# Kernel optimization log

Hardware: AMD Instinct MI355X
Metric: run time of the kernel (lower is better)

## Reference

```python
import jax, jax.numpy as jnp
import numpy as np

H = 4                      # attention heads
N_A, N_P = 20000, 30000    # author / paper node counts
E = 200000                 # edges per edge type
IN, HID, OUT = 256, 256, 128
NEG_SLOPE = 0.2


def setup_inputs() -> dict:
    key = jax.random.key(0)
    ks = jax.random.split(key, 24)

    def w(k, shape, fan_in):
        return jax.random.normal(k, shape, jnp.float32) / np.float32(np.sqrt(fan_in))

    inp = {
        'x_author': jax.random.normal(ks[0], (N_A, IN), jnp.float32),
        'x_paper':  jax.random.normal(ks[1], (N_P, IN), jnp.float32),
        'src_ap': jax.random.randint(ks[2], (E,), 0, N_A, jnp.int32),
        'dst_ap': jax.random.randint(ks[3], (E,), 0, N_P, jnp.int32),
        'src_pa': jax.random.randint(ks[4], (E,), 0, N_P, jnp.int32),
        'dst_pa': jax.random.randint(ks[5], (E,), 0, N_A, jnp.int32),
        'src_pp': jax.random.randint(ks[6], (E,), 0, N_P, jnp.int32),
        'dst_pp': jax.random.randint(ks[7], (E,), 0, N_P, jnp.int32),
        'src_aa': jax.random.randint(ks[8], (E,), 0, N_A, jnp.int32),
        'dst_aa': jax.random.randint(ks[9], (E,), 0, N_A, jnp.int32),
        # layer 1 params
        'W1_a': w(ks[10], (IN, HID), IN), 'b1_a': jnp.zeros((HID,), jnp.float32),
        'W1_p': w(ks[11], (IN, HID), IN), 'b1_p': jnp.zeros((HID,), jnp.float32),
        'att1_src': w(ks[12], (4, H, HID // H), HID // H),
        'att1_dst': w(ks[13], (4, H, HID // H), HID // H),
        'q1': w(ks[14], (HID,), HID),
        'k1_W': w(ks[15], (HID, HID), HID), 'k1_b': jnp.zeros((HID,), jnp.float32),
        # layer 2 params
        'W2_a': w(ks[16], (HID, OUT), HID), 'b2_a': jnp.zeros((OUT,), jnp.float32),
        'W2_p': w(ks[17], (HID, OUT), HID), 'b2_p': jnp.zeros((OUT,), jnp.float32),
        'att2_src': w(ks[18], (4, H, OUT // H), OUT // H),
        'att2_dst': w(ks[19], (4, H, OUT // H), OUT // H),
        'q2': w(ks[20], (OUT,), OUT),
        'k2_W': w(ks[21], (OUT, OUT), OUT), 'k2_b': jnp.zeros((OUT,), jnp.float32),
    }
    return inp


def _han_layer(h, edges, att_src, att_dst, q, kW, kb, sizes):
    """One HANConv layer. h: dict node_type -> [N, H, D]."""
    outs = {nt: [] for nt in h}
    for i, (st, dt, row, col) in enumerate(edges):
        xs, xd = h[st], h[dt]
        nd = sizes[dt]
        # per-edge additive attention logits  [E, H]
        a = jax.nn.leaky_relu((xs * att_src[i]).sum(-1)[row]
                              + (xd * att_dst[i]).sum(-1)[col], NEG_SLOPE)
        # softmax over incoming edges of each dst node (segment softmax)
        amax = jax.ops.segment_max(a, col, num_segments=nd)
        ea = jnp.exp(a - amax[col])
        denom = jax.ops.segment_sum(ea, col, num_segments=nd)
        alpha = ea / (denom[col] + 1e-16)
        # weighted scatter-sum of source features  [Nd, H, D]
        agg = jax.ops.segment_sum(xs[row] * alpha[:, :, None], col, num_segments=nd)
        outs[dt].append(jax.nn.relu(agg.reshape(nd, -1)))
    # semantic (metapath-level) attention: PyG group()
    res = {}
    for nt, lst in outs.items():
        stk = jnp.stack(lst)  # [M, N, F]
        score = (q * jnp.tanh(stk @ kW + kb).mean(axis=1)).sum(-1)  # [M]
        attn = jax.nn.softmax(score, axis=0)
        res[nt] = jnp.einsum('m,mnf->nf', attn, stk)
    return res


def reference(x_author, x_paper, src_ap, dst_ap, src_pa, dst_pa, src_pp, dst_pp,
              src_aa, dst_aa, W1_a, b1_a, W1_p, b1_p, att1_src, att1_dst, q1,
              k1_W, k1_b, W2_a, b2_a, W2_p, b2_p, att2_src, att2_dst, q2,
              k2_W, k2_b):
    sizes = {'author': N_A, 'paper': N_P}
    edges = [('author', 'paper', src_ap, dst_ap),
             ('paper', 'author', src_pa, dst_pa),
             ('paper', 'paper', src_pp, dst_pp),
             ('author', 'author', src_aa, dst_aa)]
    d1 = W1_a.shape[1] // H
    h1 = {'author': (x_author @ W1_a + b1_a).reshape(N_A, H, d1),
          'paper':  (x_paper @ W1_p + b1_p).reshape(N_P, H, d1)}
    x1 = _han_layer(h1, edges, att1_src, att1_dst, q1, k1_W, k1_b, sizes)
    d2 = W2_a.shape[1] // H
    h2 = {'author': (x1['author'] @ W2_a + b2_a).reshape(N_A, H, d2),
          'paper':  (x1['paper'] @ W2_p + b2_p).reshape(N_P, H, d2)}
    x2 = _han_layer(h2, edges, att2_src, att2_dst, q2, k2_W, k2_b, sizes)
    return x2['author']
```

## Files before the change

kernel.cpp:

```cpp
#include <hip/hip_runtime.h>
#include <math.h>


#define NA 20000
#define NP 30000
#define NE 200000
#define D1 256
#define D2 128

typedef __attribute__((ext_vector_type(8))) short short8v;
typedef __attribute__((ext_vector_type(4))) float floatx4;
typedef __attribute__((ext_vector_type(8))) unsigned short ushort8v;
typedef __attribute__((ext_vector_type(4))) unsigned short ushort4v;

static __device__ __forceinline__ float lrelu(float x) { return x >= 0.f ? x : 0.2f * x; }

static __device__ __forceinline__ unsigned short bftrunc(float x) {
    return (unsigned short)(__float_as_uint(x) >> 16);
}
static __device__ __forceinline__ float bf2f(unsigned short b) {
    return __uint_as_float(((unsigned)b) << 16);
}
static __device__ __forceinline__ unsigned short bfrn(float x) {
    unsigned u = __float_as_uint(x);
    return (unsigned short)((u + 0x7FFFu + ((u >> 16) & 1u)) >> 16);
}

typedef __attribute__((address_space(1))) const unsigned int as1_uint;
typedef __attribute__((address_space(3))) unsigned int as3_uint;
static __device__ __forceinline__ void gl_lds16(const void* g, void* l) {
    __builtin_amdgcn_global_load_lds((as1_uint*)g, (as3_uint*)l, 16, 0, 0);
}

static inline int cdiv(int a, int b) { return (a + b - 1) / b; }

struct Prologue {
    const float* W[6];
    unsigned short* img[6];
    int N[6];
    int nsl[6];
    const float* x[2];
    unsigned short* xo[2];
    int xn8[2];
    const int* dstv[4];
    int* cnt[4];
};

__global__ __launch_bounds__(256) void prologue_k(Prologue p) {
    const int task = blockIdx.y;
    const int idx = blockIdx.x * 256 + threadIdx.x;
    if (task < 6) {
        const int m = task;
        if (idx >= p.nsl[m]) return;
        const int N = p.N[m];
        const int slot = idx & 3;
        const int col = (idx >> 2) % N;
        const int rest = (idx >> 2) / N;
        const int part = rest & 1;
        const int kt = rest >> 1;
        const int ks = slot ^ ((col >> 1) & 3);
        unsigned short* dst = p.img[m] + (((size_t)(kt * 2 + part) * N + col) * 32) + slot * 8;
        const float* wsrc = p.W[m] + (size_t)(kt * 32 + ks * 8) * N + col;
        short8v o;
#pragma unroll
        for (int k = 0; k < 8; ++k) {
            const float x = wsrc[(size_t)k * N];
            const unsigned short hb = bftrunc(x);
            o[k] = part ? (short)bftrunc(x - bf2f(hb)) : (short)hb;
        }
        *(short8v*)dst = o;
    } else if (task < 8) {
        const int m = task - 6;
        if (idx >= p.xn8[m]) return;
        const float* xp = p.x[m] + (size_t)idx * 8;
        float4 v0 = *(const float4*)xp;
        float4 v1 = *(const float4*)(xp + 4);
        const float xs8[8] = {v0.x, v0.y, v0.z, v0.w, v1.x, v1.y, v1.z, v1.w};
        short8v o;
#pragma unroll
        for (int k = 0; k < 8; ++k) o[k] = (short)bfrn(xs8[k]);
        *(short8v*)&p.xo[m][(size_t)idx * 8] = o;
    } else {
        const int ty = task - 8;
        if (idx < NE) atomicAdd(&p.cnt[ty][p.dstv[ty][idx]], 1);
    }
}

struct CsrBatch {
    const int* srcv[4];
    const int* dstv[4];
    int* cnt[4];
    int* csrc[4];
    int* cdst[4];
};

__global__ __launch_bounds__(256) void fill_csr_b(CsrBatch c, int n) {
    const int ty = blockIdx.y;
    const int i = blockIdx.x * 256 + threadIdx.x;
    if (i < n) {
        const int d = c.dstv[ty][i];
        const int p = atomicAdd(&c.cnt[ty][d], 1);
        c.csrc[ty][p] = c.srcv[ty][i];
        c.cdst[ty][p] = d;
    }
}

__global__ __launch_bounds__(1024) void exscan4(int* __restrict__ curbase,
                                                int* __restrict__ rpbase) {
    const int off_c[4] = {0, NP, NP + NA, NP + NA + NP};
    const int off_r[4] = {0, NP + 1, NP + NA + 2, NP + NA + NP + 3};
    const int ns[4] = {NP, NA, NP, NA};
    const int b = blockIdx.x;
    int* cur = curbase + off_c[b];
    int* rp = rpbase + off_r[b];
    const int n = ns[b];
    __shared__ int wsum[16];
    __shared__ int carry_s;
    const int t = threadIdx.x, wv = t >> 6, ln = t & 63;
    if (t == 0) carry_s = 0;
    __syncthreads();
    for (int base = 0; base < n; base += 1024) {
        const int i = base + t;
        const int v = (i < n) ? cur[i] : 0;
        int x = v;
#pragma unroll
        for (int off = 1; off < 64; off <<= 1) {
            int y = __shfl_up(x, off);
            if (ln >= off) x += y;
        }
        if (ln == 63) wsum[wv] = x;
        __syncthreads();
        if (wv == 0) {
            int s = (ln < 16) ? wsum[ln] : 0;
#pragma unroll
            for (int off = 1; off < 16; off <<= 1) {
                int y = __shfl_up(s, off);
                if (ln >= off) s += y;
            }
            if (ln < 16) wsum[ln] = s;
        }
        __syncthreads();
        const int woff = (wv == 0) ? 0 : wsum[wv - 1];
        const int c = carry_s;
        const int ex = c + woff + x - v;
        if (i < n) { rp[i] = ex; cur[i] = ex; }
        __syncthreads();
        if (t == 1023) carry_s = c + wsum[15];
        __syncthreads();
    }
    if (t == 0) rp[n] = carry_s;
}

template <int NT>
struct GemmBatch {
    const unsigned short* A[NT];
    const unsigned short* Wimg[NT];
    const float* bias[NT];
    unsigned short* C[NT];
    int M[NT];
};

template <int BN, bool SCORE, bool SPLITW, int NT>
__global__ __launch_bounds__(256) void gemm_sw(
    GemmBatch<NT> g, const float* __restrict__ qv, float* __restrict__ score, int K) {
    constexpr int WGN = BN / 64;
    constexpr int WGM = 4 / WGN;
    constexpr int BM = WGM * 64;
    constexpr int NB = SPLITW ? 2 : 1;
    constexpr int ACH = BM * 32 * 2 / 1024;
    constexpr int BCH = NB * BN * 32 * 2 / 1024;
    constexpr int CPW = (ACH + BCH) / 4;
    constexpr int ASZ = BM * 64;
    constexpr int BSZ = NB * BN * 64;
    const int ty = blockIdx.y;
    const int M = g.M[ty];
    const int bm = blockIdx.x * BM;
    if (bm >= M) return;
    const unsigned short* __restrict__ A = g.A[ty];
    const unsigned short* __restrict__ Wi = g.Wimg[ty];
    const float* __restrict__ bias = g.bias[ty];
    __shared__ __attribute__((aligned(16))) unsigned short As[2][BM][32];
    __shared__ __attribute__((aligned(16))) unsigned short Bs[2][NB][BN][32];
    const int t = threadIdx.x;
    const int lane = t & 63, wid = t >> 6;
    const int wr = wid / WGN, wc = wid % WGN;
    const int fq = lane >> 4, fr = lane & 15;
    const int asl = (fq ^ ((fr >> 1) & 3)) * 16;
    const int lr = lane >> 2;
    const int lks = (lane & 3) ^ ((lane >> 3) & 3);
    floatx4 acc[4][4];
#pragma unroll
    for (int i = 0; i < 4; ++i)
#pragma unroll
        for (int j = 0; j < 4; ++j) acc[i][j] = {0.f, 0.f, 0.f, 0.f};

    const int NK = K >> 5;
    auto STAGE = [&](int b, int ki) {
        const char* wbase = (const char*)Wi + (size_t)ki * (2 * BN * 64);
#pragma unroll
        for (int ci = 0; ci < CPW; ++ci) {
            const int c = wid * CPW + ci;
            if (c < ACH) {
                const int row = c * 16 + lr;
                const char* srcp = (const char*)(A + (size_t)(bm + row) * K + ki * 32 + lks * 8);
                gl_lds16(srcp, (char*)As + b * ASZ + c * 1024);
            } else {
                const int bc = c - ACH;
                gl_lds16(wbase + (size_t)bc * 1024 + lane * 16, (char*)Bs + b * BSZ + bc * 1024);
            }
        }
    };
    STAGE(0, 0);
    __syncthreads();
    int cur = 0;
    for (int ki = 0; ki < NK; ++ki) {
        if (ki + 1 < NK) STAGE(cur ^ 1, ki + 1);
        short8v a[4], bh[4], bl[4];
#pragma unroll
        for (int f = 0; f < 4; ++f) {
            const int ar = wr * 64 + f * 16 + fr;
            a[f] = *(const short8v*)((const char*)As + cur * ASZ + ar * 64 + asl);
            const int bc = wc * 64 + f * 16 + fr;
            bh[f] = *(const short8v*)((const char*)Bs + cur * BSZ + bc * 64 + asl);
            if constexpr (SPLITW)
                bl[f] = *(const short8v*)((const char*)Bs + cur * BSZ + (size_t)BN * 64 + bc * 64 + asl);
        }
#pragma unroll
        for (int i = 0; i < 4; ++i)
#pragma unroll
            for (int j = 0; j < 4; ++j) {
                acc[i][j] = __builtin_amdgcn_mfma_f32_16x16x32_bf16(a[i], bh[j], acc[i][j], 0, 0, 0);
                if constexpr (SPLITW)
                    acc[i][j] = __builtin_amdgcn_mfma_f32_16x16x32_bf16(a[i], bl[j], acc[i][j], 0, 0, 0);
            }
        __syncthreads();
        cur ^= 1;
    }
    if constexpr (!SCORE) {
        unsigned short* __restrict__ Cb = g.C[ty];
#pragma unroll
        for (int i = 0; i < 4; ++i) {
            const int gr0 = bm + wr * 64 + i * 16 + fq * 4;
#pragma unroll
            for (int j = 0; j < 4; ++j) {
                const int col = wc * 64 + j * 16 + fr;
                const float b = bias[col];
#pragma unroll
                for (int r = 0; r < 4; ++r) {
                    const int gr = gr0 + r;
                    if (gr < M) Cb[(size_t)gr * BN + col] = bfrn(acc[i][j][r] + b);
                }
            }
        }
    } else {
        __shared__ float red[256];
        float partial = 0.f;
#pragma unroll
        for (int i = 0; i < 4; ++i) {
            const int gr0 = bm + wr * 64 + i * 16 + fq * 4;
#pragma unroll
            for (int j = 0; j < 4; ++j) {
                const int col = wc * 64 + j * 16 + fr;
                const float b = bias[col], q = qv[col];
#pragma unroll
                for (int r = 0; r < 4; ++r) {
                    if (gr0 + r < M) partial += tanhf(acc[i][j][r] + b) * q;
                }
            }
        }
        red[t] = partial;
        __syncthreads();
        for (int s = 128; s > 0; s >>= 1) {
            if (t < s) red[t] += red[t + s];
            __syncthreads();
        }
        if (t == 0) atomicAdd(&score[ty], red[0]);
    }
}

struct NsBatch {
    const unsigned short* hx[2];
    const float* att[2][4];
    float* out[2][4];
    int n[2];
    int nsc[2];
};

template <int HD>
__global__ __launch_bounds__(256) void ns_b(NsBatch p) {
    const int ty = blockIdx.y;
    const int idx = blockIdx.x * 256 + threadIdx.x;
    const int node = idx >> 2, hh = idx & 3;
    if (node >= p.n[ty]) return;
    const unsigned short* row = p.hx[ty] + (size_t)node * (4 * HD) + hh * HD;
    const int nsc = p.nsc[ty];
    float s[4] = {0.f, 0.f, 0.f, 0.f};
#pragma unroll
    for (int d = 0; d < HD; d += 4) {
        ushort4v xv = *(const ushort4v*)&row[d];
        const float x0 = bf2f(xv[0]), x1 = bf2f(xv[1]), x2 = bf2f(xv[2]), x3 = bf2f(xv[3]);
#pragma unroll
        for (int v = 0; v < 4; ++v) {
            if (v < nsc) {
                float4 a = *(const float4*)&p.att[ty][v][hh * HD + d];
                s[v] += x0 * a.x + x1 * a.y + x2 * a.z + x3 * a.w;
            }
        }
    }
#pragma unroll
    for (int v = 0; v < 4; ++v)
        if (v < nsc) p.out[ty][v][idx] = s[v];
}

template <int EPL>
static __device__ __forceinline__ void accum(const unsigned short* p, float ea, float* acc) {
    if constexpr (EPL >= 8) {
#pragma unroll
        for (int w = 0; w < EPL / 8; ++w) {
            ushort8v x = *(const ushort8v*)(p + w * 8);
#pragma unroll
            for (int k = 0; k < 8; ++k) acc[w * 8 + k] += bf2f(x[k]) * ea;
        }
    } else {
        ushort4v x = *(const ushort4v*)p;
#pragma unroll
        for (int k = 0; k < 4; ++k) acc[k] += bf2f(x[k]) * ea;
    }
}

template <int NT>
struct AggBatch {
    const unsigned short* xs[NT];
    const float* ss[NT];
    const float* sd[NT];
    const int* csrc[NT];
    const int* rowptr[NT];
    unsigned short* out[NT];
    int ndst[NT];
};

template <int D, int NT>
__global__ __launch_bounds__(256) void agg_b(AggBatch<NT> a) {
    constexpr int EPL = D / 32;
    const int ty = blockIdx.y;
    const int gid = blockIdx.x * 8 + (threadIdx.x >> 5);
    if (gid >= a.ndst[ty]) return;
    const int g = threadIdx.x & 31;
    const int h = g >> 3;
    const int* __restrict__ rp = a.rowptr[ty];
    const int e0 = rp[gid], e1 = rp[gid + 1];
    const float* __restrict__ ss = a.ss[ty];
    const int* __restrict__ cs = a.csrc[ty];
    const unsigned short* __restrict__ xs = a.xs[ty];
    const float sdh = a.sd[ty][gid * 4 + h];
    float acc[EPL] = {};
    float denom = 0.f;
    int e = e0;
    for (; e + 4 <= e1; e += 4) {
        const int r0 = cs[e], r1 = cs[e + 1], r2 = cs[e + 2], r3 = cs[e + 3];
        const float l0 = lrelu(ss[r0 * 4 + h] + sdh);
        const float l1 = lrelu(ss[r1 * 4 + h] + sdh);
        const float l2 = lrelu(ss[r2 * 4 + h] + sdh);
        const float l3 = lrelu(ss[r3 * 4 + h] + sdh);
        const float ea0 = __expf(l0), ea1 = __expf(l1);
        const float ea2 = __expf(l2), ea3 = __expf(l3);
        denom += (ea0 + ea1) + (ea2 + ea3);
        accum<EPL>(xs + (size_t)r0 * D + g * EPL, ea0, acc);
        accum<EPL>(xs + (size_t)r1 * D + g * EPL, ea1, acc);
        accum<EPL>(xs + (size_t)r2 * D + g * EPL, ea2, acc);
        accum<EPL>(xs + (size_t)r3 * D + g * EPL, ea3, acc);
    }
    for (; e < e1; ++e) {
        const int r0 = cs[e];
        const float l0 = lrelu(ss[r0 * 4 + h] + sdh);
        const float ea0 = __expf(l0);
        denom += ea0;
        accum<EPL>(xs + (size_t)r0 * D + g * EPL, ea0, acc);
    }
    const float inv = 1.f / (denom + 1e-16f);
    unsigned short* __restrict__ orow = a.out[ty] + (size_t)gid * D + g * EPL;
    if constexpr (EPL >= 8) {
#pragma unroll
        for (int w = 0; w < EPL / 8; ++w) {
            short8v o;
#pragma unroll
            for (int k = 0; k < 8; ++k)
                o[k] = (short)bfrn(fmaxf(acc[w * 8 + k] * inv, 0.f));
            *(short8v*)&orow[w * 8] = o;
        }
    } else {
        ushort4v o;
#pragma unroll
        for (int k = 0; k < 4; ++k)
            o[k] = bfrn(fmaxf(acc[k] * inv, 0.f));
        *(ushort4v*)orow = o;
    }
}

struct CombBatch {
    const unsigned short* a[2];
    const unsigned short* b[2];
    unsigned short* o[2];
    int n8[2];
    int slot[2];
    float invN[2];
};

__global__ __launch_bounds__(256) void combine_b(CombBatch c, const float* __restrict__ sc) {
    const int ty = blockIdx.y;
    const int i = blockIdx.x * 256 + threadIdx.x;
    if (i >= c.n8[ty]) return;
    const float s0 = sc[c.slot[ty]] * c.invN[ty];
    const float s1 = sc[c.slot[ty] + 1] * c.invN[ty];
    const float m = fmaxf(s0, s1);
    const float e0 = expf(s0 - m), e1 = expf(s1 - m);
    const float w0 = e0 / (e0 + e1), w1 = e1 / (e0 + e1);
    const size_t o = (size_t)i * 8;
    ushort8v x = *(const ushort8v*)&c.a[ty][o];
    ushort8v y = *(const ushort8v*)&c.b[ty][o];
    short8v r;
#pragma unroll
    for (int k = 0; k < 8; ++k)
        r[k] = (short)bfrn(w0 * bf2f(x[k]) + w1 * bf2f(y[k]));
    *(short8v*)&c.o[ty][o] = r;
}

__global__ __launch_bounds__(256) void combine_out(
    const unsigned short* __restrict__ a, const unsigned short* __restrict__ b,
    float* __restrict__ out, const float* __restrict__ sc, int slot, float invN, int n8) {
    const int i = blockIdx.x * 256 + threadIdx.x;
    if (i >= n8) return;
    const float s0 = sc[slot] * invN, s1 = sc[slot + 1] * invN;
    const float m = fmaxf(s0, s1);
    const float e0 = expf(s0 - m), e1 = expf(s1 - m);
    const float w0 = e0 / (e0 + e1), w1 = e1 / (e0 + e1);
    const size_t o = (size_t)i * 8;
    ushort8v x = *(const ushort8v*)&a[o];
    ushort8v y = *(const ushort8v*)&b[o];
    float rr[8];
#pragma unroll
    for (int k = 0; k < 8; ++k) rr[k] = w0 * bf2f(x[k]) + w1 * bf2f(y[k]);
    float4 r0 = {rr[0], rr[1], rr[2], rr[3]};
    float4 r1 = {rr[4], rr[5], rr[6], rr[7]};
    *(float4*)&out[o] = r0;
    *(float4*)&out[o + 4] = r1;
}

extern "C" void kernel_launch(void* const* d_in, const int* in_sizes, int n_in,
                              void* d_out, int out_size, void* d_ws, size_t ws_size,
                              hipStream_t stream) {
    const float* x_a = (const float*)d_in[0];
    const float* x_p = (const float*)d_in[1];
    const int* src[4] = {(const int*)d_in[2], (const int*)d_in[4], (const int*)d_in[6], (const int*)d_in[8]};
    const int* dst[4] = {(const int*)d_in[3], (const int*)d_in[5], (const int*)d_in[7], (const int*)d_in[9]};
    const float* W1a = (const float*)d_in[10]; const float* b1a = (const float*)d_in[11];
    const float* W1p = (const float*)d_in[12]; const float* b1p = (const float*)d_in[13];
    const float* att1s = (const float*)d_in[14]; const float* att1d = (const float*)d_in[15];
    const float* q1 = (const float*)d_in[16];
    const float* k1W = (const float*)d_in[17]; const float* k1b = (const float*)d_in[18];
    const float* W2a = (const float*)d_in[19]; const float* b2a = (const float*)d_in[20];
    const float* W2p = (const float*)d_in[21]; const float* b2p = (const float*)d_in[22];
    const float* att2s = (const float*)d_in[23]; const float* att2d = (const float*)d_in[24];
    const float* q2 = (const float*)d_in[25];
    const float* k2W = (const float*)d_in[26]; const float* k2b = (const float*)d_in[27];

    const int NAp = NA + 128, NPp = NP + 128;
    char* wp = (char*)d_ws;
    unsigned short* xa_bf = (unsigned short*)wp; wp += (size_t)NAp * D1 * 2;
    unsigned short* xp_bf = (unsigned short*)wp; wp += (size_t)NPp * D1 * 2;
    unsigned short* h1a_bf = (unsigned short*)wp; wp += (size_t)NA * D1 * 2;
    unsigned short* h1p_bf = (unsigned short*)wp; wp += (size_t)NP * D1 * 2;
    unsigned short* a0 = (unsigned short*)wp; wp += (size_t)NPp * D1 * 2;
    unsigned short* a1 = (unsigned short*)wp; wp += (size_t)NAp * D1 * 2;
    unsigned short* a2 = (unsigned short*)wp; wp += (size_t)NPp * D1 * 2;
    unsigned short* a3 = (unsigned short*)wp; wp += (size_t)NAp * D1 * 2;
    float* sv = (float*)wp; wp += (size_t)(16 * NA + 16 * NP) * 4;
    int* rp_base = (int*)wp; wp += (size_t)(NP + NA + NP + NA + 4) * 4;
    int* cur_base = (int*)wp; wp += (size_t)(NP + NA + NP + NA) * 4;
    float* sc = (float*)wp; wp += 16 * 4;
    int* csrc_base = (int*)wp; wp += (size_t)4 * NE * 4;
    int* cdst_base = (int*)wp; wp += (size_t)4 * NE * 4;
    unsigned short* img_w1a = (unsigned short*)wp; wp += (size_t)8 * 2 * 256 * 32 * 2;
    unsigned short* img_w1p = (unsigned short*)wp; wp += (size_t)8 * 2 * 256 * 32 * 2;
    unsigned short* img_k1w = (unsigned short*)wp; wp += (size_t)8 * 2 * 256 * 32 * 2;
    unsigned short* img_w2a = (unsigned short*)wp; wp += (size_t)8 * 2 * 128 * 32 * 2;
    unsigned short* img_w2p = (unsigned short*)wp; wp += (size_t)8 * 2 * 128 * 32 * 2;
    unsigned short* img_k2w = (unsigned short*)wp; wp += (size_t)4 * 2 * 128 * 32 * 2;
    const size_t need_bytes = (size_t)(wp - (char*)d_ws);
    if (ws_size < need_bytes) return;

    int* rp[4] = {rp_base, rp_base + NP + 1, rp_base + NP + NA + 2, rp_base + NP + NA + NP + 3};
    int* cur[4] = {cur_base, cur_base + NP, cur_base + NP + NA, cur_base + NP + NA + NP};
    int* csrc[4]; int* cdst[4];
    for (int i = 0; i < 4; ++i) {
        csrc[i] = csrc_base + (size_t)i * NE;
        cdst[i] = cdst_base + (size_t)i * NE;
    }
    float* ss0 = sv;             float* sd0 = ss0 + NA * 4;
    float* ss1 = sd0 + NP * 4;   float* sd1 = ss1 + NP * 4;
    float* ss2 = sd1 + NA * 4;   float* sd2 = ss2 + NP * 4;
    float* ss3 = sd2 + NP * 4;   float* sd3 = ss3 + NA * 4;
    unsigned short* res_p = a0;
    unsigned short* res_a = a1;
    unsigned short* h2a_bf = a2;
    unsigned short* h2p_bf = a2 + (size_t)NA * D2;
    unsigned short* g21 = a3;
    unsigned short* g23 = a3 + (size_t)NAp * D2;
    float* ss21 = sv;             float* sd21 = ss21 + NP * 4;
    float* ss23 = sd21 + NA * 4;  float* sd23 = ss23 + NA * 4;

    hipMemsetAsync(cur_base, 0, (size_t)(NP + NA + NP + NA) * sizeof(int) + 16 * sizeof(float), stream);

    Prologue pl;
    const float* Ws[6] = {W1a, W1p, k1W, W2a, W2p, k2W};
    unsigned short* imgs[6] = {img_w1a, img_w1p, img_k1w, img_w2a, img_w2p, img_k2w};
    const int Ns[6] = {256, 256, 256, 128, 128, 128};
    const int nsls[6] = {8 * 2 * 256 * 4, 8 * 2 * 256 * 4, 8 * 2 * 256 * 4,
                         8 * 2 * 128 * 4, 8 * 2 * 128 * 4, 4 * 2 * 128 * 4};
    for (int i = 0; i < 6; ++i) { pl.W[i] = Ws[i]; pl.img[i] = imgs[i]; pl.N[i] = Ns[i]; pl.nsl[i] = nsls[i]; }
    pl.x[0] = x_a; pl.x[1] = x_p;
    pl.xo[0] = xa_bf; pl.xo[1] = xp_bf;
    pl.xn8[0] = NA * D1 / 8; pl.xn8[1] = NP * D1 / 8;
    for (int i = 0; i < 4; ++i) { pl.dstv[i] = dst[i]; pl.cnt[i] = cur[i]; }
    prologue_k<<<dim3(cdiv(NP * D1 / 8, 256), 12), 256, 0, stream>>>(pl);

    exscan4<<<4, 1024, 0, stream>>>(cur_base, rp_base);
    CsrBatch cb;
    for (int i = 0; i < 4; ++i) {
        cb.srcv[i] = src[i]; cb.dstv[i] = dst[i];
        cb.cnt[i] = cur[i]; cb.csrc[i] = csrc[i]; cb.cdst[i] = cdst[i];
    }
    fill_csr_b<<<dim3(cdiv(NE, 256), 4), 256, 0, stream>>>(cb, NE);

    GemmBatch<2> t1 = {{xa_bf, xp_bf}, {img_w1a, img_w1p}, {b1a, b1p}, {h1a_bf, h1p_bf}, {NA, NP}};
    gemm_sw<256, false, true, 2><<<dim3(cdiv(NP, 64), 2), 256, 0, stream>>>(t1, nullptr, nullptr, 256);

    NsBatch n1;
    n1.hx[0] = h1a_bf; n1.hx[1] = h1p_bf;
    n1.att[0][0] = att1s + 0 * 256; n1.att[0][1] = att1d + 1 * 256;
    n1.att[0][2] = att1s + 3 * 256; n1.att[0][3] = att1d + 3 * 256;
    n1.att[1][0] = att1d + 0 * 256; n1.att[1][1] = att1s + 1 * 256;
    n1.att[1][2] = att1s + 2 * 256; n1.att[1][3] = att1d + 2 * 256;
    n1.out[0][0] = ss0; n1.out[0][1] = sd1; n1.out[0][2] = ss3; n1.out[0][3] = sd3;
    n1.out[1][0] = sd0; n1.out[1][1] = ss1; n1.out[1][2] = ss2; n1.out[1][3] = sd2;
    n1.n[0] = NA; n1.n[1] = NP; n1.nsc[0] = 4; n1.nsc[1] = 4;
    ns_b<64><<<dim3(cdiv(NP * 4, 256), 2), 256, 0, stream>>>(n1);

    AggBatch<4> ab1 = {{h1a_bf, h1p_bf, h1p_bf, h1a_bf},
                       {ss0, ss1, ss2, ss3}, {sd0, sd1, sd2, sd3},
                       {csrc[0], csrc[1], csrc[2], csrc[3]},
                       {rp[0], rp[1], rp[2], rp[3]},
                       {a0, a1, a2, a3},
                       {NP, NA, NP, NA}};
    agg_b<256, 4><<<dim3(cdiv(NP, 8), 4), 256, 0, stream>>>(ab1);

    GemmBatch<4> s1 = {{a0, a2, a1, a3},
                       {img_k1w, img_k1w, img_k1w, img_k1w},
                       {k1b, k1b, k1b, k1b},
                       {nullptr, nullptr, nullptr, nullptr},
                       {NP, NP, NA, NA}};
    gemm_sw<256, true, false, 4><<<dim3(cdiv(NP, 64), 4), 256, 0, stream>>>(s1, q1, sc, 256);
    CombBatch c1 = {{a0, a1}, {a2, a3}, {res_p, res_a},
                    {NP * D1 / 8, NA * D1 / 8}, {0, 2}, {1.f / NP, 1.f / NA}};
    combine_b<<<dim3(cdiv(NP * D1 / 8, 256), 2), 256, 0, stream>>>(c1, sc);

    GemmBatch<2> t2 = {{res_a, res_p}, {img_w2a, img_w2p}, {b2a, b2p}, {h2a_bf, h2p_bf}, {NA, NP}};
    gemm_sw<128, false, true, 2><<<dim3(cdiv(NP, 128), 2), 256, 0, stream>>>(t2, nullptr, nullptr, 256);

    NsBatch n2;
    n2.hx[0] = h2a_bf; n2.hx[1] = h2p_bf;
    n2.att[0][0] = att2d + 1 * 128; n2.att[0][1] = att2s + 3 * 128;
    n2.att[0][2] = att2d + 3 * 128; n2.att[0][3] = nullptr;
    n2.att[1][0] = att2s + 1 * 128; n2.att[1][1] = nullptr;
    n2.att[1][2] = nullptr; n2.att[1][3] = nullptr;
    n2.out[0][0] = sd21; n2.out[0][1] = ss23; n2.out[0][2] = sd23; n2.out[0][3] = nullptr;
    n2.out[1][0] = ss21; n2.out[1][1] = nullptr; n2.out[1][2] = nullptr; n2.out[1][3] = nullptr;
    n2.n[0] = NA; n2.n[1] = NP; n2.nsc[0] = 3; n2.nsc[1] = 1;
    ns_b<32><<<dim3(cdiv(NP * 4, 256), 2), 256, 0, stream>>>(n2);

    AggBatch<2> ab2 = {{h2p_bf, h2a_bf},
                       {ss21, ss23}, {sd21, sd23},
                       {csrc[1], csrc[3]}, {rp[1], rp[3]},
                       {g21, g23}, {NA, NA}};
    agg_b<128, 2><<<dim3(cdiv(NA, 8), 2), 256, 0, stream>>>(ab2);

    GemmBatch<2> s2 = {{g21, g23}, {img_k2w, img_k2w}, {k2b, k2b}, {nullptr, nullptr}, {NA, NA}};
    gemm_sw<128, true, false, 2><<<dim3(cdiv(NA, 128), 2), 256, 0, stream>>>(s2, q2, sc + 4, 128);
    combine_out<<<cdiv(NA * D2 / 8, 256), 256, 0, stream>>>(
        g21, g23, (float*)d_out, sc, 4, 1.f / NA, NA * D2 / 8);
}
```

Before: 400.7 us.

## Fuse node attention scores into projection GEMM epilogue and pack aggregation FMAs

Node-level attention dot products (ns_b) are now computed in the projection GEMM epilogue from fp32 accumulators, using cross-lane shuffles per head, so the separate kernel and its re-read of the bf16 projections are removed. Separately, the edge aggregation accumulates in float2 vectors to encourage packed FMA instructions. The epilogue adds shuffle work and register pressure to the GEMM, and the scores now come from unrounded fp32 values rather than from the bf16 outputs.

```diff
diff --git a/kernel.cpp b/kernel.cpp
--- a/kernel.cpp
+++ b/kernel.cpp
@@ -10,6 +10,7 @@
 
 typedef __attribute__((ext_vector_type(8))) short short8v;
 typedef __attribute__((ext_vector_type(4))) float floatx4;
+typedef __attribute__((ext_vector_type(2))) float float2v;
 typedef __attribute__((ext_vector_type(8))) unsigned short ushort8v;
 typedef __attribute__((ext_vector_type(4))) unsigned short ushort4v;
 
@@ -158,9 +159,12 @@
     const float* bias[NT];
     unsigned short* C[NT];
     int M[NT];
+    const float* att[NT][4];
+    float* sout[NT][4];
+    int nsc[NT];
 };
 
-template <int BN, bool SCORE, bool SPLITW, int NT>
+template <int BN, bool SCORE, bool SPLITW, bool NSF, int NT>
 __global__ __launch_bounds__(256) void gemm_sw(
     GemmBatch<NT> g, const float* __restrict__ qv, float* __restrict__ score, int K) {
     constexpr int WGN = BN / 64;
@@ -252,6 +256,50 @@
                 }
             }
         }
+        if constexpr (NSF) {
+            const int nscv = g.nsc[ty];
+            float bj[4];
+#pragma unroll
+            for (int j = 0; j < 4; ++j) bj[j] = bias[wc * 64 + j * 16 + fr];
+#pragma unroll
+            for (int v = 0; v < 4; ++v) {
+                if (v >= nscv) break;
+                const float* __restrict__ av = g.att[ty][v];
+                float* __restrict__ sv = g.sout[ty][v];
+                float avj[4];
+#pragma unroll
+                for (int j = 0; j < 4; ++j) avj[j] = av[wc * 64 + j * 16 + fr];
+#pragma unroll
+                for (int i = 0; i < 4; ++i) {
+#pragma unroll
+                    for (int r = 0; r < 4; ++r) {
+                        const int gr = bm + wr * 64 + i * 16 + fq * 4 + r;
+                        if constexpr (BN == 256) {
+                            float pr = 0.f;
+#pragma unroll
+                            for (int j = 0; j < 4; ++j)
+                                pr += (acc[i][j][r] + bj[j]) * avj[j];
+                            pr += __shfl_xor(pr, 1); pr += __shfl_xor(pr, 2);
+                            pr += __shfl_xor(pr, 4); pr += __shfl_xor(pr, 8);
+                            if (fr == 0 && gr < M) sv[gr * 4 + wc] = pr;
+                        } else {
+                            float p0 = (acc[i][0][r] + bj[0]) * avj[0]
+                                     + (acc[i][1][r] + bj[1]) * avj[1];
+                            float p1 = (acc[i][2][r] + bj[2]) * avj[2]
+                                     + (acc[i][3][r] + bj[3]) * avj[3];
+                            p0 += __shfl_xor(p0, 1); p0 += __shfl_xor(p0, 2);
+                            p0 += __shfl_xor(p0, 4); p0 += __shfl_xor(p0, 8);
+                            p1 += __shfl_xor(p1, 1); p1 += __shfl_xor(p1, 2);
+                            p1 += __shfl_xor(p1, 4); p1 += __shfl_xor(p1, 8);
+                            if (fr == 0 && gr < M) {
+                                sv[gr * 4 + 2 * wc] = p0;
+                                sv[gr * 4 + 2 * wc + 1] = p1;
+                            }
+                        }
+                    }
+                }
+            }
+        }
     } else {
         __shared__ float red[256];
         float partial = 0.f;
@@ -278,53 +326,26 @@
     }
 }
 
-struct NsBatch {
-    const unsigned short* hx[2];
-    const float* att[2][4];
-    float* out[2][4];
-    int n[2];
-    int nsc[2];
-};
-
-template <int HD>
-__global__ __launch_bounds__(256) void ns_b(NsBatch p) {
-    const int ty = blockIdx.y;
-    const int idx = blockIdx.x * 256 + threadIdx.x;
-    const int node = idx >> 2, hh = idx & 3;
-    if (node >= p.n[ty]) return;
-    const unsigned short* row = p.hx[ty] + (size_t)node * (4 * HD) + hh * HD;
-    const int nsc = p.nsc[ty];
-    float s[4] = {0.f, 0.f, 0.f, 0.f};
-#pragma unroll
-    for (int d = 0; d < HD; d += 4) {
-        ushort4v xv = *(const ushort4v*)&row[d];
-        const float x0 = bf2f(xv[0]), x1 = bf2f(xv[1]), x2 = bf2f(xv[2]), x3 = bf2f(xv[3]);
-#pragma unroll
-        for (int v = 0; v < 4; ++v) {
-            if (v < nsc) {
-                float4 a = *(const float4*)&p.att[ty][v][hh * HD + d];
-                s[v] += x0 * a.x + x1 * a.y + x2 * a.z + x3 * a.w;
-            }
-        }
-    }
-#pragma unroll
-    for (int v = 0; v < 4; ++v)
-        if (v < nsc) p.out[ty][v][idx] = s[v];
-}
-
 template <int EPL>
-static __device__ __forceinline__ void accum(const unsigned short* p, float ea, float* acc) {
+static __device__ __forceinline__ void accum(const unsigned short* p, float ea, float2v* acc2) {
+    const float2v eav = {ea, ea};
     if constexpr (EPL >= 8) {
 #pragma unroll
         for (int w = 0; w < EPL / 8; ++w) {
             ushort8v x = *(const ushort8v*)(p + w * 8);
 #pragma unroll
-            for (int k = 0; k < 8; ++k) acc[w * 8 + k] += bf2f(x[k]) * ea;
+            for (int k = 0; k < 4; ++k) {
+                float2v xv = {bf2f(x[2 * k]), bf2f(x[2 * k + 1])};
+                acc2[w * 4 + k] += xv * eav;
+            }
         }
     } else {
         ushort4v x = *(const ushort4v*)p;
 #pragma unroll
-        for (int k = 0; k < 4; ++k) acc[k] += bf2f(x[k]) * ea;
+        for (int k = 0; k < 2; ++k) {
+            float2v xv = {bf2f(x[2 * k]), bf2f(x[2 * k + 1])};
+            acc2[k] += xv * eav;
+        }
     }
 }
 
@@ -353,7 +374,9 @@
     const int* __restrict__ cs = a.csrc[ty];
     const unsigned short* __restrict__ xs = a.xs[ty];
     const float sdh = a.sd[ty][gid * 4 + h];
-    float acc[EPL] = {};
+    float2v acc2[EPL / 2];
+#pragma unroll
+    for (int k = 0; k < EPL / 2; ++k) acc2[k] = {0.f, 0.f};
     float denom = 0.f;
     int e = e0;
     for (; e + 4 <= e1; e += 4) {
@@ -365,17 +388,17 @@
         const float ea0 = __expf(l0), ea1 = __expf(l1);
         const float ea2 = __expf(l2), ea3 = __expf(l3);
         denom += (ea0 + ea1) + (ea2 + ea3);
-        accum<EPL>(xs + (size_t)r0 * D + g * EPL, ea0, acc);
-        accum<EPL>(xs + (size_t)r1 * D + g * EPL, ea1, acc);
-        accum<EPL>(xs + (size_t)r2 * D + g * EPL, ea2, acc);
-        accum<EPL>(xs + (size_t)r3 * D + g * EPL, ea3, acc);
+        accum<EPL>(xs + (size_t)r0 * D + g * EPL, ea0, acc2);
+        accum<EPL>(xs + (size_t)r1 * D + g * EPL, ea1, acc2);
+        accum<EPL>(xs + (size_t)r2 * D + g * EPL, ea2, acc2);
+        accum<EPL>(xs + (size_t)r3 * D + g * EPL, ea3, acc2);
     }
     for (; e < e1; ++e) {
         const int r0 = cs[e];
         const float l0 = lrelu(ss[r0 * 4 + h] + sdh);
         const float ea0 = __expf(l0);
         denom += ea0;
-        accum<EPL>(xs + (size_t)r0 * D + g * EPL, ea0, acc);
+        accum<EPL>(xs + (size_t)r0 * D + g * EPL, ea0, acc2);
     }
     const float inv = 1.f / (denom + 1e-16f);
     unsigned short* __restrict__ orow = a.out[ty] + (size_t)gid * D + g * EPL;
@@ -384,15 +407,19 @@
         for (int w = 0; w < EPL / 8; ++w) {
             short8v o;
 #pragma unroll
-            for (int k = 0; k < 8; ++k)
-                o[k] = (short)bfrn(fmaxf(acc[w * 8 + k] * inv, 0.f));
+            for (int k = 0; k < 4; ++k) {
+                o[2 * k] = (short)bfrn(fmaxf(acc2[w * 4 + k][0] * inv, 0.f));
+                o[2 * k + 1] = (short)bfrn(fmaxf(acc2[w * 4 + k][1] * inv, 0.f));
+            }
             *(short8v*)&orow[w * 8] = o;
         }
     } else {
         ushort4v o;
 #pragma unroll
-        for (int k = 0; k < 4; ++k)
-            o[k] = bfrn(fmaxf(acc[k] * inv, 0.f));
+        for (int k = 0; k < 2; ++k) {
+            o[2 * k] = bfrn(fmaxf(acc2[k][0] * inv, 0.f));
+            o[2 * k + 1] = bfrn(fmaxf(acc2[k][1] * inv, 0.f));
+        }
         *(ushort4v*)orow = o;
     }
 }
@@ -532,19 +559,20 @@
     }
     fill_csr_b<<<dim3(cdiv(NE, 256), 4), 256, 0, stream>>>(cb, NE);
 
-    GemmBatch<2> t1 = {{xa_bf, xp_bf}, {img_w1a, img_w1p}, {b1a, b1p}, {h1a_bf, h1p_bf}, {NA, NP}};
-    gemm_sw<256, false, true, 2><<<dim3(cdiv(NP, 64), 2), 256, 0, stream>>>(t1, nullptr, nullptr, 256);
-
-    NsBatch n1;
-    n1.hx[0] = h1a_bf; n1.hx[1] = h1p_bf;
-    n1.att[0][0] = att1s + 0 * 256; n1.att[0][1] = att1d + 1 * 256;
-    n1.att[0][2] = att1s + 3 * 256; n1.att[0][3] = att1d + 3 * 256;
-    n1.att[1][0] = att1d + 0 * 256; n1.att[1][1] = att1s + 1 * 256;
-    n1.att[1][2] = att1s + 2 * 256; n1.att[1][3] = att1d + 2 * 256;
-    n1.out[0][0] = ss0; n1.out[0][1] = sd1; n1.out[0][2] = ss3; n1.out[0][3] = sd3;
-    n1.out[1][0] = sd0; n1.out[1][1] = ss1; n1.out[1][2] = ss2; n1.out[1][3] = sd2;
-    n1.n[0] = NA; n1.n[1] = NP; n1.nsc[0] = 4; n1.nsc[1] = 4;
-    ns_b<64><<<dim3(cdiv(NP * 4, 256), 2), 256, 0, stream>>>(n1);
+    GemmBatch<2> t1;
+    t1.A[0] = xa_bf; t1.A[1] = xp_bf;
+    t1.Wimg[0] = img_w1a; t1.Wimg[1] = img_w1p;
+    t1.bias[0] = b1a; t1.bias[1] = b1p;
+    t1.C[0] = h1a_bf; t1.C[1] = h1p_bf;
+    t1.M[0] = NA; t1.M[1] = NP;
+    t1.att[0][0] = att1s + 0 * 256; t1.att[0][1] = att1d + 1 * 256;
+    t1.att[0][2] = att1s + 3 * 256; t1.att[0][3] = att1d + 3 * 256;
+    t1.att[1][0] = att1d + 0 * 256; t1.att[1][1] = att1s + 1 * 256;
+    t1.att[1][2] = att1s + 2 * 256; t1.att[1][3] = att1d + 2 * 256;
+    t1.sout[0][0] = ss0; t1.sout[0][1] = sd1; t1.sout[0][2] = ss3; t1.sout[0][3] = sd3;
+    t1.sout[1][0] = sd0; t1.sout[1][1] = ss1; t1.sout[1][2] = ss2; t1.sout[1][3] = sd2;
+    t1.nsc[0] = 4; t1.nsc[1] = 4;
+    gemm_sw<256, false, true, true, 2><<<dim3(cdiv(NP, 64), 2), 256, 0, stream>>>(t1, nullptr, nullptr, 256);
 
     AggBatch<4> ab1 = {{h1a_bf, h1p_bf, h1p_bf, h1a_bf},
                        {ss0, ss1, ss2, ss3}, {sd0, sd1, sd2, sd3},
@@ -554,29 +582,32 @@
                        {NP, NA, NP, NA}};
     agg_b<256, 4><<<dim3(cdiv(NP, 8), 4), 256, 0, stream>>>(ab1);
 
-    GemmBatch<4> s1 = {{a0, a2, a1, a3},
-                       {img_k1w, img_k1w, img_k1w, img_k1w},
-                       {k1b, k1b, k1b, k1b},
-                       {nullptr, nullptr, nullptr, nullptr},
-                       {NP, NP, NA, NA}};
-    gemm_sw<256, true, false, 4><<<dim3(cdiv(NP, 64), 4), 256, 0, stream>>>(s1, q1, sc, 256);
+    GemmBatch<4> s1;
+    s1.A[0] = a0; s1.A[1] = a2; s1.A[2] = a1; s1.A[3] = a3;
+    s1.Wimg[0] = s1.Wimg[1] = s1.Wimg[2] = s1.Wimg[3] = img_k1w;
+    s1.bias[0] = s1.bias[1] = s1.bias[2] = s1.bias[3] = k1b;
+    s1.C[0] = s1.C[1] = s1.C[2] = s1.C[3] = nullptr;
+    s1.M[0] = NP; s1.M[1] = NP; s1.M[2] = NA; s1.M[3] = NA;
+    s1.nsc[0] = s1.nsc[1] = s1.nsc[2] = s1.nsc[3] = 0;
+    gemm_sw<256, true, false, false, 4><<<dim3(cdiv(NP, 64), 4), 256, 0, stream>>>(s1, q1, sc, 256);
     CombBatch c1 = {{a0, a1}, {a2, a3}, {res_p, res_a},
                     {NP * D1 / 8, NA * D1 / 8}, {0, 2}, {1.f / NP, 1.f / NA}};
     combine_b<<<dim3(cdiv(NP * D1 / 8, 256), 2), 256, 0, stream>>>(c1, sc);
 
-    GemmBatch<2> t2 = {{res_a, res_p}, {img_w2a, img_w2p}, {b2a, b2p}, {h2a_bf, h2p_bf}, {NA, NP}};
-    gemm_sw<128, false, true, 2><<<dim3(cdiv(NP, 128), 2), 256, 0, stream>>>(t2, nullptr, nullptr, 256);
-
-    NsBatch n2;
-    n2.hx[0] = h2a_bf; n2.hx[1] = h2p_bf;
-    n2.att[0][0] = att2d + 1 * 128; n2.att[0][1] = att2s + 3 * 128;
-    n2.att[0][2] = att2d + 3 * 128; n2.att[0][3] = nullptr;
-    n2.att[1][0] = att2s + 1 * 128; n2.att[1][1] = nullptr;
-    n2.att[1][2] = nullptr; n2.att[1][3] = nullptr;
-    n2.out[0][0] = sd21; n2.out[0][1] = ss23; n2.out[0][2] = sd23; n2.out[0][3] = nullptr;
-    n2.out[1][0] = ss21; n2.out[1][1] = nullptr; n2.out[1][2] = nullptr; n2.out[1][3] = nullptr;
-    n2.n[0] = NA; n2.n[1] = NP; n2.nsc[0] = 3; n2.nsc[1] = 1;
-    ns_b<32><<<dim3(cdiv(NP * 4, 256), 2), 256, 0, stream>>>(n2);
+    GemmBatch<2> t2;
+    t2.A[0] = res_a; t2.A[1] = res_p;
+    t2.Wimg[0] = img_w2a; t2.Wimg[1] = img_w2p;
+    t2.bias[0] = b2a; t2.bias[1] = b2p;
+    t2.C[0] = h2a_bf; t2.C[1] = h2p_bf;
+    t2.M[0] = NA; t2.M[1] = NP;
+    t2.att[0][0] = att2d + 1 * 128; t2.att[0][1] = att2s + 3 * 128;
+    t2.att[0][2] = att2d + 3 * 128; t2.att[0][3] = nullptr;
+    t2.att[1][0] = att2s + 1 * 128; t2.att[1][1] = nullptr;
+    t2.att[1][2] = nullptr; t2.att[1][3] = nullptr;
+    t2.sout[0][0] = sd21; t2.sout[0][1] = ss23; t2.sout[0][2] = sd23; t2.sout[0][3] = nullptr;
+    t2.sout[1][0] = ss21; t2.sout[1][1] = nullptr; t2.sout[1][2] = nullptr; t2.sout[1][3] = nullptr;
+    t2.nsc[0] = 3; t2.nsc[1] = 1;
+    gemm_sw<128, false, true, true, 2><<<dim3(cdiv(NP, 128), 2), 256, 0, stream>>>(t2, nullptr, nullptr, 256);
 
     AggBatch<2> ab2 = {{h2p_bf, h2a_bf},
                        {ss21, ss23}, {sd21, sd23},
@@ -584,8 +615,14 @@
                        {g21, g23}, {NA, NA}};
     agg_b<128, 2><<<dim3(cdiv(NA, 8), 2), 256, 0, stream>>>(ab2);
 
-    GemmBatch<2> s2 = {{g21, g23}, {img_k2w, img_k2w}, {k2b, k2b}, {nullptr, nullptr}, {NA, NA}};
-    gemm_sw<128, true, false, 2><<<dim3(cdiv(NA, 128), 2), 256, 0, stream>>>(s2, q2, sc + 4, 128);
+    GemmBatch<2> s2;
+    s2.A[0] = g21; s2.A[1] = g23;
+    s2.Wimg[0] = s2.Wimg[1] = img_k2w;
+    s2.bias[0] = s2.bias[1] = k2b;
+    s2.C[0] = s2.C[1] = nullptr;
+    s2.M[0] = NA; s2.M[1] = NA;
+    s2.nsc[0] = s2.nsc[1] = 0;
+    gemm_sw<128, true, false, false, 2><<<dim3(cdiv(NA, 128), 2), 256, 0, stream>>>(s2, q2, sc + 4, 128);
     combine_out<<<cdiv(NA * D2 / 8, 256), 256, 0, stream>>>(
         g21, g23, (float*)d_out, sc, 4, 1.f / NA, NA * D2 / 8);
 }
```

After: 367.3 us. -8.4%, faster.
